# Kernel optimization log

Hardware: AMD Instinct MI355X
Metric: run time of the kernel (lower is better)

Reference implementation:

```python
import jax, jax.numpy as jnp
import numpy as np

N_NODES = 100000
N_EDGES = 3200000
IN_DIM = 64
HID = 64


def setup_inputs() -> dict:
    key = jax.random.key(0)
    ks = jax.random.split(key, 12)
    x = jax.random.normal(ks[0], (N_NODES, IN_DIM), dtype=jnp.float32)
    edge_index = jax.random.randint(ks[1], (2, N_EDGES), 0, N_NODES, dtype=jnp.int64)
    tau = jax.random.uniform(ks[2], (N_NODES, 1), dtype=jnp.float32)
    d1 = IN_DIM + 1  # augmented feature dim
    s1 = 1.0 / np.sqrt(d1)
    s2 = 1.0 / np.sqrt(HID)
    # SAGEConv: out = lin_l(mean_aggr) + lin_r(x); bias lives in lin_l. Weights stored [in, out].
    W1l = jax.random.uniform(ks[3], (d1, HID), jnp.float32, -s1, s1)
    b1l = jax.random.uniform(ks[4], (HID,), jnp.float32, -s1, s1)
    W1r = jax.random.uniform(ks[5], (d1, HID), jnp.float32, -s1, s1)
    W2l = jax.random.uniform(ks[6], (HID, HID), jnp.float32, -s2, s2)
    b2l = jax.random.uniform(ks[7], (HID,), jnp.float32, -s2, s2)
    W2r = jax.random.uniform(ks[8], (HID, HID), jnp.float32, -s2, s2)
    Wfc = jax.random.uniform(ks[9], (HID, 1), jnp.float32, -s2, s2)
    bfc = jax.random.uniform(ks[10], (1,), jnp.float32, -s2, s2)
    return {"x": x, "edge_index": edge_index, "tau": tau,
            "W1l": W1l, "b1l": b1l, "W1r": W1r,
            "W2l": W2l, "b2l": b2l, "W2r": W2r,
            "Wfc": Wfc, "bfc": bfc}


def _sage_conv(x, src, dst, Wl, bl, Wr, n_nodes):
    # mean aggregation of source-node features onto target nodes
    summed = jax.ops.segment_sum(x[src], dst, num_segments=n_nodes)  # [N, d]
    deg = jax.ops.segment_sum(jnp.ones(src.shape[0], x.dtype), dst, num_segments=n_nodes)
    mean = summed / jnp.maximum(deg, 1.0)[:, None]
    return mean @ Wl + bl + x @ Wr


def reference(x, edge_index, tau, W1l, b1l, W1r, W2l, b2l, W2r, Wfc, bfc):
    src, dst = edge_index[0], edge_index[1]
    n = x.shape[0]
    h = jnp.concatenate([x, tau], axis=1)  # augment_features: append tau column
    h = jax.nn.relu(_sage_conv(h, src, dst, W1l, b1l, W1r, n))
    h = jax.nn.relu(_sage_conv(h, src, dst, W2l, b2l, W2r, n))
    return h @ Wfc + bfc  # [N, 1]
```

## Files before the change

### kernel.cpp

```cpp
#include <hip/hip_runtime.h>
#include <hip/hip_bf16.h>
#include <hip/hip_fp16.h>
#include <hip/hip_fp8.h>


#define BSH 7
#define NBKT 782
#define NBLK 512
#define PER 6250
#define CAP 6144
#define ABLK 512

typedef _Float16 half8 __attribute__((ext_vector_type(8)));
typedef float floatx4 __attribute__((ext_vector_type(4)));
typedef float floatx2 __attribute__((ext_vector_type(2)));

struct h4s { __half2 lo, hi; };

#if __has_builtin(__builtin_amdgcn_cvt_pk_f32_fp8)
template <bool HI>
__device__ __forceinline__ float2 f8x2_to_f2(int v) {
    floatx2 r = __builtin_amdgcn_cvt_pk_f32_fp8(v, HI);
    return make_float2(r.x, r.y);
}
#else
template <bool HI>
__device__ __forceinline__ float2 f8x2_to_f2(int v) {
    unsigned short u = HI ? (unsigned short)(((unsigned)v) >> 16)
                          : (unsigned short)(v & 0xFFFF);
    __half2_raw r = __hip_cvt_fp8x2_to_halfraw2((__hip_fp8x2_storage_t)u, __HIP_E4M3);
    return __half22float2(*(__half2*)&r);
}
#endif

#if __has_builtin(__builtin_amdgcn_cvt_pk_fp8_f32)
__device__ __forceinline__ unsigned f4_to_f8x4(float a, float b, float c, float d) {
    int lo = __builtin_amdgcn_cvt_pk_fp8_f32(a, b, 0, false);
    return (unsigned)__builtin_amdgcn_cvt_pk_fp8_f32(c, d, lo, true);
}
__device__ __forceinline__ unsigned char f_to_f8(float a) {
    return (unsigned char)(__builtin_amdgcn_cvt_pk_fp8_f32(a, a, 0, false) & 0xFF);
}
#else
__device__ __forceinline__ unsigned f4_to_f8x4(float a, float b, float c, float d) {
    unsigned lo = (unsigned)__hip_cvt_float2_to_fp8x2(make_float2(a, b), __HIP_SATFINITE, __HIP_E4M3);
    unsigned hi = (unsigned)__hip_cvt_float2_to_fp8x2(make_float2(c, d), __HIP_SATFINITE, __HIP_E4M3);
    return lo | (hi << 16);
}
__device__ __forceinline__ unsigned char f_to_f8(float a) {
    return (unsigned char)__hip_cvt_float_to_fp8(a, __HIP_SATFINITE, __HIP_E4M3);
}
#endif

__global__ __launch_bounds__(256) void k_histprep(
    const int* __restrict__ dst, int* __restrict__ histT, int E,
    const float* __restrict__ x, __half* __restrict__ xh,
    unsigned char* __restrict__ xf8, int n4,
    const float* __restrict__ W1l, const float* __restrict__ W1r,
    const float* __restrict__ W2l, const float* __restrict__ W2r,
    __half* __restrict__ wbuf1, __half* __restrict__ wbuf2) {
    if (blockIdx.x < NBLK) {
        __shared__ int h[NBKT];
        for (int i = threadIdx.x; i < NBKT; i += 256) h[i] = 0;
        __syncthreads();
        int lo = blockIdx.x * PER;
        int hi = lo + PER; if (hi > E) hi = E;
        for (int e = lo + threadIdx.x; e < hi; e += 256)
            atomicAdd(&h[dst[e] >> BSH], 1);
        __syncthreads();
        for (int k = threadIdx.x; k < NBKT; k += 256)
            histT[k * NBLK + blockIdx.x] = h[k];
    } else if (blockIdx.x < NBLK + 9) {
        int idx = (blockIdx.x - NBLK) * 256 + threadIdx.x;
        if (idx < 1280) {
            int lane = idx & 63;
            int nt = (idx >> 6) & 3;
            int kstep = idx >> 8;
            int col = nt * 16 + (lane & 15);
            int kbase = kstep * 32 + (lane >> 4) * 8;
#pragma unroll
            for (int j = 0; j < 8; ++j) {
                int k = kbase + j;
                float v;
                if (k < 64)        v = W1l[k * 64 + col];
                else if (k < 128)  v = W1r[(k - 64) * 64 + col];
                else if (k == 128) v = W1l[64 * 64 + col];
                else if (k == 129) v = W1r[64 * 64 + col];
                else v = 0.f;
                wbuf1[(size_t)idx * 8 + j] = __float2half(v);
            }
        } else if (idx < 1280 + 1024) {
            int i2 = idx - 1280;
            int lane = i2 & 63;
            int nt = (i2 >> 6) & 3;
            int kstep = i2 >> 8;
            int col = nt * 16 + (lane & 15);
            int kbase = kstep * 32 + (lane >> 4) * 8;
#pragma unroll
            for (int j = 0; j < 8; ++j) {
                int k = kbase + j;
                float v = (k < 64) ? W2l[k * 64 + col] : W2r[(k - 64) * 64 + col];
                wbuf2[(size_t)i2 * 8 + j] = __float2half(v);
            }
        }
    } else {
        int i = (blockIdx.x - NBLK - 9) * 256 + threadIdx.x;
        if (i < n4) {
            float4 v = ((const float4*)x)[i];
            ((__half2*)xh)[2 * i]     = __floats2half2_rn(v.x, v.y);
            ((__half2*)xh)[2 * i + 1] = __floats2half2_rn(v.z, v.w);
            ((unsigned*)xf8)[i] = f4_to_f8x4(v.x, v.y, v.z, v.w);
        }
    }
}


__global__ __launch_bounds__(NBLK) void k_scanblk(int* __restrict__ histT,
                                                  int* __restrict__ btot) {
    __shared__ int s[NBLK];
    int k = blockIdx.x, t = threadIdx.x;
    int v = histT[k * NBLK + t];
    s[t] = v;
    __syncthreads();
    for (int off = 1; off < NBLK; off <<= 1) {
        int u = (t >= off) ? s[t - off] : 0;
        __syncthreads();
        s[t] += u;
        __syncthreads();
    }
    histT[k * NBLK + t] = s[t] - v;
    if (t == NBLK - 1) btot[k] = s[t];
}

__global__ __launch_bounds__(1024) void k_scanbkt(const int* __restrict__ btot,
                                                  int* __restrict__ bstart) {
    __shared__ int s[1024];
    int t = threadIdx.x;
    int v = (t < NBKT) ? btot[t] : 0;
    s[t] = v;
    __syncthreads();
    for (int off = 1; off < 1024; off <<= 1) {
        int u = (t >= off) ? s[t - off] : 0;
        __syncthreads();
        s[t] += u;
        __syncthreads();
    }
    if (t < NBKT) bstart[t] = s[t] - v;
    if (t == NBKT - 1) bstart[NBKT] = s[t];
}

__global__ __launch_bounds__(256) void k_scatter(const int* __restrict__ src,
                                                 const int* __restrict__ dst,
                                                 const int* __restrict__ histT,
                                                 const int* __restrict__ bstart,
                                                 int* __restrict__ binned, int E) {
    __shared__ int sorted[PER];
    __shared__ int lstart[NBKT + 1];
    __shared__ int cur[NBKT];
    __shared__ int gst[NBKT];
    __shared__ int tsum[256];
    int b = blockIdx.x, t = threadIdx.x;
    int base = b * PER;
    int blen = E - base; if (blen > PER) blen = PER;

    for (int k = t; k < NBKT; k += 256) lstart[k] = 0;
    __syncthreads();
    for (int e = base + t; e < base + blen; e += 256)
        atomicAdd(&lstart[dst[e] >> BSH], 1);
    __syncthreads();
    int c0 = 0;
    int i0 = t * 4;
#pragma unroll
    for (int j = 0; j < 4; ++j)
        if (i0 + j < NBKT) c0 += lstart[i0 + j];
    tsum[t] = c0;
    __syncthreads();
    for (int off = 1; off < 256; off <<= 1) {
        int u = (t >= off) ? tsum[t - off] : 0;
        __syncthreads();
        tsum[t] += u;
        __syncthreads();
    }
    int running = tsum[t] - c0;
    __syncthreads();
#pragma unroll
    for (int j = 0; j < 4; ++j) {
        int i = i0 + j;
        if (i < NBKT) {
            int v = lstart[i];
            lstart[i] = running;
            running += v;
        }
    }
    __syncthreads();
    if (t == 0) lstart[NBKT] = blen;
    for (int k = t; k < NBKT; k += 256) {
        cur[k] = lstart[k];
        gst[k] = bstart[k] + histT[k * NBLK + b];
    }
    __syncthreads();
    for (int e = base + t; e < base + blen; e += 256) {
        int d = dst[e], s = src[e];
        int pos = atomicAdd(&cur[d >> BSH], 1);
        sorted[pos] = (s << BSH) | (d & ((1 << BSH) - 1));
    }
    __syncthreads();
    int qw = t >> 4, ql = t & 15;
    for (int k = qw; k < NBKT; k += 16) {
        int st = lstart[k];
        int ln = lstart[k + 1] - st;
        int gd = gst[k];
        for (int i = ql; i < ln; i += 16)
            binned[gd + i] = sorted[st + i];
    }
}


__global__ __launch_bounds__(ABLK) void k_aggrb1(
    const int* __restrict__ binned, const int* __restrict__ bstart,
    const unsigned char* __restrict__ xf8, const float* __restrict__ tau,
    __half* __restrict__ zm1, __half* __restrict__ mt1, int N) {
    __shared__ int cidx[CAP];
    __shared__ int cnt[128], s[128], cur[128];
    int k = blockIdx.x, t = threadIdx.x;
    int lo = bstart[k], hi = bstart[k + 1];
    if (t < 128) cnt[t] = 0;
    __syncthreads();
    for (int e = lo + t; e < hi; e += ABLK)
        atomicAdd(&cnt[binned[e] & 127], 1);
    __syncthreads();
    if (t < 128) s[t] = cnt[t];
    __syncthreads();
    for (int off = 1; off < 128; off <<= 1) {
        int u = 0;
        if (t < 128 && t >= off) u = s[t - off];
        __syncthreads();
        if (t < 128) s[t] += u;
        __syncthreads();
    }
    if (t < 128) cur[t] = s[t] - cnt[t];
    __syncthreads();
    for (int e = lo + t; e < hi; e += ABLK) {
        int p = binned[e];
        int pos = atomicAdd(&cur[p & 127], 1);
        if (pos < CAP) cidx[pos] = p >> BSH;
    }
    __syncthreads();

    int lane = t & 63;
    int q = lane >> 4;
    int c = lane & 15;
    int qb = lane & 48;
    int g = c & 3;
    int ch = c >> 2;
    unsigned cb = (unsigned)(ch << 4);
    int bpl = (qb + g) << 2;
    const char* xb = (const char*)xf8;

    for (int p = (t >> 6); p < 32; p += (ABLK / 64)) {
        int ld = (p << 2) + q;
        int node = (k << BSH) + ld;
        int d = cnt[ld];
        int startL = cur[ld] - d;
        int dm = d;
        dm = max(dm, __shfl_xor(dm, 16, 64));
        dm = max(dm, __shfl_xor(dm, 32, 64));
        float4 A0 = {0.f, 0.f, 0.f, 0.f}, A1 = A0, A2 = A0, A3 = A0;
        float sumtau = 0.f;
        for (int base = 0; base < dm; base += 16) {
            int n = d - base;
            n = (n < 0) ? 0 : (n > 16 ? 16 : n);
            int nmax = dm - base; if (nmax > 16) nmax = 16;
            int ng = (nmax + 3) >> 2;
            int sidx = 0;
            if (c < n) {
                int ii = startL + base + c;
                if (ii >= CAP) ii = 0;
                sidx = cidx[ii];
                sumtau += tau[sidx];
            }
            int4 r0, r1, r2, r3;
            int i0 = __builtin_amdgcn_ds_bpermute(bpl, sidx);
            r0 = *(const int4*)(xb + (((unsigned)i0 << 6) + cb));
            if (ng > 1) {
                int i1 = __builtin_amdgcn_ds_bpermute(bpl + 16, sidx);
                r1 = *(const int4*)(xb + (((unsigned)i1 << 6) + cb));
            }
            if (ng > 2) {
                int i2 = __builtin_amdgcn_ds_bpermute(bpl + 32, sidx);
                r2 = *(const int4*)(xb + (((unsigned)i2 << 6) + cb));
            }
            if (ng > 3) {
                int i3 = __builtin_amdgcn_ds_bpermute(bpl + 48, sidx);
                r3 = *(const int4*)(xb + (((unsigned)i3 << 6) + cb));
            }
            auto accum = [&](const int4& r) {
                float2 l0 = f8x2_to_f2<false>(r.x), h0 = f8x2_to_f2<true>(r.x);
                float2 l1 = f8x2_to_f2<false>(r.y), h1v = f8x2_to_f2<true>(r.y);
                float2 l2 = f8x2_to_f2<false>(r.z), h2v = f8x2_to_f2<true>(r.z);
                float2 l3 = f8x2_to_f2<false>(r.w), h3v = f8x2_to_f2<true>(r.w);
                A0.x += l0.x; A0.y += l0.y; A0.z += h0.x; A0.w += h0.y;
                A1.x += l1.x; A1.y += l1.y; A1.z += h1v.x; A1.w += h1v.y;
                A2.x += l2.x; A2.y += l2.y; A2.z += h2v.x; A2.w += h2v.y;
                A3.x += l3.x; A3.y += l3.y; A3.z += h3v.x; A3.w += h3v.y;
            };
            if (g < n)                accum(r0);
            if (ng > 1 && 4 + g < n)  accum(r1);
            if (ng > 2 && 8 + g < n)  accum(r2);
            if (ng > 3 && 12 + g < n) accum(r3);
        }
#pragma unroll
        for (int off = 1; off <= 2; off <<= 1) {
            A0.x += __shfl_xor(A0.x, off, 64); A0.y += __shfl_xor(A0.y, off, 64);
            A0.z += __shfl_xor(A0.z, off, 64); A0.w += __shfl_xor(A0.w, off, 64);
            A1.x += __shfl_xor(A1.x, off, 64); A1.y += __shfl_xor(A1.y, off, 64);
            A1.z += __shfl_xor(A1.z, off, 64); A1.w += __shfl_xor(A1.w, off, 64);
            A2.x += __shfl_xor(A2.x, off, 64); A2.y += __shfl_xor(A2.y, off, 64);
            A2.z += __shfl_xor(A2.z, off, 64); A2.w += __shfl_xor(A2.w, off, 64);
            A3.x += __shfl_xor(A3.x, off, 64); A3.y += __shfl_xor(A3.y, off, 64);
            A3.z += __shfl_xor(A3.z, off, 64); A3.w += __shfl_xor(A3.w, off, 64);
        }
#pragma unroll
        for (int off = 8; off > 0; off >>= 1) sumtau += __shfl_xor(sumtau, off, 64);

        float inv = 1.f / fmaxf((float)d, 1.f);
        if (node < N) {
            float4 Aw = (g == 0) ? A0 : ((g == 1) ? A1 : ((g == 2) ? A2 : A3));
            h4s o;
            o.lo = __floats2half2_rn(Aw.x * inv, Aw.y * inv);
            o.hi = __floats2half2_rn(Aw.z * inv, Aw.w * inv);
            *(h4s*)(zm1 + (size_t)node * 64 + (ch << 4) + (g << 2)) = o;
            if (c == 0) mt1[node] = __float2half(sumtau * inv);
        }
    }
}

__global__ __launch_bounds__(ABLK) void k_aggrb2(
    const int* __restrict__ binned, const int* __restrict__ bstart,
    const unsigned char* __restrict__ h1f8, __half* __restrict__ zm2, int N) {
    __shared__ int cidx[CAP];
    __shared__ int cnt[128], s[128], cur[128];
    int k = blockIdx.x, t = threadIdx.x;
    int lo = bstart[k], hi = bstart[k + 1];
    if (t < 128) cnt[t] = 0;
    __syncthreads();
    for (int e = lo + t; e < hi; e += ABLK)
        atomicAdd(&cnt[binned[e] & 127], 1);
    __syncthreads();
    if (t < 128) s[t] = cnt[t];
    __syncthreads();
    for (int off = 1; off < 128; off <<= 1) {
        int u = 0;
        if (t < 128 && t >= off) u = s[t - off];
        __syncthreads();
        if (t < 128) s[t] += u;
        __syncthreads();
    }
    if (t < 128) cur[t] = s[t] - cnt[t];
    __syncthreads();
    for (int e = lo + t; e < hi; e += ABLK) {
        int p = binned[e];
        int pos = atomicAdd(&cur[p & 127], 1);
        if (pos < CAP) cidx[pos] = p >> BSH;
    }
    __syncthreads();

    int lane = t & 63;
    int q = lane >> 4;
    int c = lane & 15;
    int qb = lane & 48;
    int g = c & 3;
    int ch = c >> 2;
    unsigned cb = (unsigned)(ch << 4);
    int bpl = (qb + g) << 2;
    const char* hb = (const char*)h1f8;

    for (int p = (t >> 6); p < 32; p += (ABLK / 64)) {
        int ld = (p << 2) + q;
        int node = (k << BSH) + ld;
        int d = cnt[ld];
        int startL = cur[ld] - d;
        int dm = d;
        dm = max(dm, __shfl_xor(dm, 16, 64));
        dm = max(dm, __shfl_xor(dm, 32, 64));
        float4 A0 = {0.f, 0.f, 0.f, 0.f}, A1 = A0, A2 = A0, A3 = A0;
        for (int base = 0; base < dm; base += 16) {
            int n = d - base;
            n = (n < 0) ? 0 : (n > 16 ? 16 : n);
            int nmax = dm - base; if (nmax > 16) nmax = 16;
            int ng = (nmax + 3) >> 2;
            int sidx = 0;
            if (c < n) {
                int ii = startL + base + c;
                if (ii >= CAP) ii = 0;
                sidx = cidx[ii];
            }
            int4 r0, r1, r2, r3;
            int i0 = __builtin_amdgcn_ds_bpermute(bpl, sidx);
            r0 = *(const int4*)(hb + (((unsigned)i0 << 6) + cb));
            if (ng > 1) {
                int i1 = __builtin_amdgcn_ds_bpermute(bpl + 16, sidx);
                r1 = *(const int4*)(hb + (((unsigned)i1 << 6) + cb));
            }
            if (ng > 2) {
                int i2 = __builtin_amdgcn_ds_bpermute(bpl + 32, sidx);
                r2 = *(const int4*)(hb + (((unsigned)i2 << 6) + cb));
            }
            if (ng > 3) {
                int i3 = __builtin_amdgcn_ds_bpermute(bpl + 48, sidx);
                r3 = *(const int4*)(hb + (((unsigned)i3 << 6) + cb));
            }
            auto accum = [&](const int4& r) {
                float2 l0 = f8x2_to_f2<false>(r.x), h0 = f8x2_to_f2<true>(r.x);
                float2 l1 = f8x2_to_f2<false>(r.y), h1v = f8x2_to_f2<true>(r.y);
                float2 l2 = f8x2_to_f2<false>(r.z), h2v = f8x2_to_f2<true>(r.z);
                float2 l3 = f8x2_to_f2<false>(r.w), h3v = f8x2_to_f2<true>(r.w);
                A0.x += l0.x; A0.y += l0.y; A0.z += h0.x; A0.w += h0.y;
                A1.x += l1.x; A1.y += l1.y; A1.z += h1v.x; A1.w += h1v.y;
                A2.x += l2.x; A2.y += l2.y; A2.z += h2v.x; A2.w += h2v.y;
                A3.x += l3.x; A3.y += l3.y; A3.z += h3v.x; A3.w += h3v.y;
            };
            if (g < n)                accum(r0);
            if (ng > 1 && 4 + g < n)  accum(r1);
            if (ng > 2 && 8 + g < n)  accum(r2);
            if (ng > 3 && 12 + g < n) accum(r3);
        }
#pragma unroll
        for (int off = 1; off <= 2; off <<= 1) {
            A0.x += __shfl_xor(A0.x, off, 64); A0.y += __shfl_xor(A0.y, off, 64);
            A0.z += __shfl_xor(A0.z, off, 64); A0.w += __shfl_xor(A0.w, off, 64);
            A1.x += __shfl_xor(A1.x, off, 64); A1.y += __shfl_xor(A1.y, off, 64);
            A1.z += __shfl_xor(A1.z, off, 64); A1.w += __shfl_xor(A1.w, off, 64);
            A2.x += __shfl_xor(A2.x, off, 64); A2.y += __shfl_xor(A2.y, off, 64);
            A2.z += __shfl_xor(A2.z, off, 64); A2.w += __shfl_xor(A2.w, off, 64);
            A3.x += __shfl_xor(A3.x, off, 64); A3.y += __shfl_xor(A3.y, off, 64);
            A3.z += __shfl_xor(A3.z, off, 64); A3.w += __shfl_xor(A3.w, off, 64);
        }
        float inv = 1.f / fmaxf((float)d, 1.f);
        if (node < N) {
            float4 Aw = (g == 0) ? A0 : ((g == 1) ? A1 : ((g == 2) ? A2 : A3));
            h4s o;
            o.lo = __floats2half2_rn(Aw.x * inv, Aw.y * inv);
            o.hi = __floats2half2_rn(Aw.z * inv, Aw.w * inv);
            *(h4s*)(zm2 + (size_t)node * 64 + (ch << 4) + (g << 2)) = o;
        }
    }
}


__global__ __launch_bounds__(256) void k_gemm1(
    const __half* __restrict__ zm1, const __half* __restrict__ mt1,
    const __half* __restrict__ xh, const float* __restrict__ tau,
    const __half* __restrict__ wbuf1, const float* __restrict__ b1l,
    __half* __restrict__ h1, unsigned char* __restrict__ h1f8, int ntiles) {
    int tile = blockIdx.x * 4 + (threadIdx.x >> 6);
    if (tile >= ntiles) return;
    int lane = threadIdx.x & 63;
    int sub = lane & 15;
    int quad = lane >> 4;
    int row = tile * 16 + sub;

    floatx4 acc0 = {0.f, 0.f, 0.f, 0.f};
    floatx4 acc1 = {0.f, 0.f, 0.f, 0.f};
    floatx4 acc2 = {0.f, 0.f, 0.f, 0.f};
    floatx4 acc3 = {0.f, 0.f, 0.f, 0.f};

    const _Float16* zrow = (const _Float16*)zm1 + (size_t)row * 64 + quad * 8;
    const _Float16* xrow = (const _Float16*)xh + (size_t)row * 64 + quad * 8;
    const _Float16* wb = (const _Float16*)wbuf1 + (size_t)lane * 8;

    half8 amat[5];
    amat[0] = *(const half8*)(zrow);
    amat[1] = *(const half8*)(zrow + 32);
    amat[2] = *(const half8*)(xrow);
    amat[3] = *(const half8*)(xrow + 32);
    half8 a4 = {0, 0, 0, 0, 0, 0, 0, 0};
    if (quad == 0) {
        a4[0] = ((const _Float16*)mt1)[row];
        a4[1] = (_Float16)tau[row];
    }
    amat[4] = a4;

#pragma unroll
    for (int ks = 0; ks < 5; ++ks) {
        half8 a = amat[ks];
        half8 b0 = *(const half8*)(wb + (size_t)(ks * 4 + 0) * 512);
        half8 b1 = *(const half8*)(wb + (size_t)(ks * 4 + 1) * 512);
        half8 b2 = *(const half8*)(wb + (size_t)(ks * 4 + 2) * 512);
        half8 b3 = *(const half8*)(wb + (size_t)(ks * 4 + 3) * 512);
        acc0 = __builtin_amdgcn_mfma_f32_16x16x32_f16(a, b0, acc0, 0, 0, 0);
        acc1 = __builtin_amdgcn_mfma_f32_16x16x32_f16(a, b1, acc1, 0, 0, 0);
        acc2 = __builtin_amdgcn_mfma_f32_16x16x32_f16(a, b2, acc2, 0, 0, 0);
        acc3 = __builtin_amdgcn_mfma_f32_16x16x32_f16(a, b3, acc3, 0, 0, 0);
    }
    float bv0 = b1l[sub], bv1 = b1l[16 + sub], bv2 = b1l[32 + sub], bv3 = b1l[48 + sub];
#pragma unroll
    for (int reg = 0; reg < 4; ++reg) {
        int r = quad * 4 + reg;
        float v0 = fmaxf(acc0[reg] + bv0, 0.f);
        float v1 = fmaxf(acc1[reg] + bv1, 0.f);
        float v2 = fmaxf(acc2[reg] + bv2, 0.f);
        float v3 = fmaxf(acc3[reg] + bv3, 0.f);
        __half* orow = h1 + (size_t)(tile * 16 + r) * 64;
        orow[sub]      = __float2half(v0);
        orow[16 + sub] = __float2half(v1);
        orow[32 + sub] = __float2half(v2);
        orow[48 + sub] = __float2half(v3);
        unsigned char* orow8 = h1f8 + (size_t)(tile * 16 + r) * 64;
        orow8[sub]      = f_to_f8(v0);
        orow8[16 + sub] = f_to_f8(v1);
        orow8[32 + sub] = f_to_f8(v2);
        orow8[48 + sub] = f_to_f8(v3);
    }
}

__global__ __launch_bounds__(256) void k_gemm2(
    const __half* __restrict__ zm2, const __half* __restrict__ h1,
    const __half* __restrict__ wbuf2, const float* __restrict__ b2l,
    const float* __restrict__ Wfc, const float* __restrict__ bfc,
    float* __restrict__ out, int ntiles) {
    int tile = blockIdx.x * 4 + (threadIdx.x >> 6);
    if (tile >= ntiles) return;
    int lane = threadIdx.x & 63;
    int sub = lane & 15;
    int quad = lane >> 4;
    int row = tile * 16 + sub;

    floatx4 acc0 = {0.f, 0.f, 0.f, 0.f};
    floatx4 acc1 = {0.f, 0.f, 0.f, 0.f};
    floatx4 acc2 = {0.f, 0.f, 0.f, 0.f};
    floatx4 acc3 = {0.f, 0.f, 0.f, 0.f};

    const _Float16* zrow = (const _Float16*)zm2 + (size_t)row * 64 + quad * 8;
    const _Float16* hrow = (const _Float16*)h1 + (size_t)row * 64 + quad * 8;
    const _Float16* wb = (const _Float16*)wbuf2 + (size_t)lane * 8;

    half8 amat[4];
    amat[0] = *(const half8*)(zrow);
    amat[1] = *(const half8*)(zrow + 32);
    amat[2] = *(const half8*)(hrow);
    amat[3] = *(const half8*)(hrow + 32);

#pragma unroll
    for (int ks = 0; ks < 4; ++ks) {
        half8 a = amat[ks];
        half8 b0 = *(const half8*)(wb + (size_t)(ks * 4 + 0) * 512);
        half8 b1 = *(const half8*)(wb + (size_t)(ks * 4 + 1) * 512);
        half8 b2 = *(const half8*)(wb + (size_t)(ks * 4 + 2) * 512);
        half8 b3 = *(const half8*)(wb + (size_t)(ks * 4 + 3) * 512);
        acc0 = __builtin_amdgcn_mfma_f32_16x16x32_f16(a, b0, acc0, 0, 0, 0);
        acc1 = __builtin_amdgcn_mfma_f32_16x16x32_f16(a, b1, acc1, 0, 0, 0);
        acc2 = __builtin_amdgcn_mfma_f32_16x16x32_f16(a, b2, acc2, 0, 0, 0);
        acc3 = __builtin_amdgcn_mfma_f32_16x16x32_f16(a, b3, acc3, 0, 0, 0);
    }
    float bb0 = b2l[sub], bb1 = b2l[16 + sub], bb2 = b2l[32 + sub], bb3 = b2l[48 + sub];
    float wv0 = Wfc[sub], wv1 = Wfc[16 + sub], wv2 = Wfc[32 + sub], wv3 = Wfc[48 + sub];
    float p[4];
#pragma unroll
    for (int reg = 0; reg < 4; ++reg) {
        p[reg] = fmaxf(acc0[reg] + bb0, 0.f) * wv0
               + fmaxf(acc1[reg] + bb1, 0.f) * wv1
               + fmaxf(acc2[reg] + bb2, 0.f) * wv2
               + fmaxf(acc3[reg] + bb3, 0.f) * wv3;
    }
#pragma unroll
    for (int m = 1; m <= 8; m <<= 1) {
#pragma unroll
        for (int reg = 0; reg < 4; ++reg) p[reg] += __shfl_xor(p[reg], m, 64);
    }
    if (sub == 0) {
        float b0 = bfc[0];
#pragma unroll
        for (int reg = 0; reg < 4; ++reg)
            out[tile * 16 + quad * 4 + reg] = p[reg] + b0;
    }
}

extern "C" void kernel_launch(void* const* d_in, const int* in_sizes, int n_in,
                              void* d_out, int out_size, void* d_ws, size_t ws_size,
                              hipStream_t stream) {
    const float* x   = (const float*)d_in[0];
    const int*   ei  = (const int*)d_in[1];
    const float* tau = (const float*)d_in[2];
    const float* W1l = (const float*)d_in[3];
    const float* b1l = (const float*)d_in[4];
    const float* W1r = (const float*)d_in[5];
    const float* W2l = (const float*)d_in[6];
    const float* b2l = (const float*)d_in[7];
    const float* W2r = (const float*)d_in[8];
    const float* Wfc = (const float*)d_in[9];
    const float* bfc = (const float*)d_in[10];
    float* out = (float*)d_out;

    const int N = in_sizes[0] / 64;
    const int E = in_sizes[1] / 2;
    const int* src = ei;
    const int* dst = ei + E;

    char* w = (char*)d_ws;
    auto take = [&](size_t b) { char* p = w; w += (b + 255) & ~(size_t)255; return p; };
    int*           histT  = (int*)take((size_t)NBKT * NBLK * 4);
    int*           btot   = (int*)take((size_t)NBKT * 4);
    int*           bstart = (int*)take((size_t)(NBKT + 1) * 4);
    int*           binned = (int*)take((size_t)E * 4);
    __half*        xh     = (__half*)take((size_t)N * 64 * 2);
    unsigned char* xf8    = (unsigned char*)take((size_t)N * 64);
    __half*        h1     = (__half*)take((size_t)N * 64 * 2);
    unsigned char* h1f8   = (unsigned char*)take((size_t)N * 64);
    __half*        zm1    = (__half*)take((size_t)N * 64 * 2);
    __half*        mt1    = (__half*)take((size_t)N * 2);
    __half*        zm2    = (__half*)take((size_t)N * 64 * 2);
    __half*        wbuf1  = (__half*)take(1280 * 8 * 2);
    __half*        wbuf2  = (__half*)take(1024 * 8 * 2);

    int n4 = N * 16;
    int hpblocks = NBLK + 9 + (n4 + 255) / 256;
    int ntiles = N / 16;
    int gblocks = (ntiles + 3) / 4;

    k_histprep<<<hpblocks, 256, 0, stream>>>(dst, histT, E, x, xh, xf8, n4,
                                             W1l, W1r, W2l, W2r, wbuf1, wbuf2);
    k_scanblk <<<NBKT, NBLK, 0, stream>>>(histT, btot);
    k_scanbkt <<<1, 1024, 0, stream>>>(btot, bstart);
    k_scatter <<<NBLK, 256, 0, stream>>>(src, dst, histT, bstart, binned, E);
    k_aggrb1  <<<NBKT, ABLK, 0, stream>>>(binned, bstart, xf8, tau, zm1, mt1, N);
    k_gemm1   <<<gblocks, 256, 0, stream>>>(zm1, mt1, xh, tau, wbuf1, b1l, h1, h1f8, ntiles);
    k_aggrb2  <<<NBKT, ABLK, 0, stream>>>(binned, bstart, h1f8, zm2, N);
    k_gemm2   <<<gblocks, 256, 0, stream>>>(zm2, h1, wbuf2, b2l, Wfc, bfc, out, ntiles);
}
```

Baseline: 276.8 us.

## Split each aggregation bucket across two half-blocks and drop bpermute index broadcast

Each 128-node bucket in both aggregation kernels is now handled by two 256-thread blocks, each taking 64 nodes and keeping a smaller shared index buffer. This gives more, smaller blocks for load balance and occupancy. The cost is that both blocks scan the full bucket edge list and filter by node half. Lanes now read their neighbour indices straight from shared memory instead of through a ds_bpermute broadcast, and the tau sum is done by the first column group with a shorter shuffle reduction.

```diff
diff --git a/kernel.cpp b/kernel.cpp
--- a/kernel.cpp
+++ b/kernel.cpp
@@ -8,8 +8,8 @@
 #define NBKT 782
 #define NBLK 512
 #define PER 6250
-#define CAP 6144
-#define ABLK 512
+#define CAPH 3072
+#define AB2 256
 
 typedef _Float16 half8 __attribute__((ext_vector_type(8)));
 typedef float floatx4 __attribute__((ext_vector_type(4)));
@@ -216,50 +216,52 @@
 }
 
 
-__global__ __launch_bounds__(ABLK) void k_aggrb1(
+__global__ __launch_bounds__(AB2) void k_aggrb1(
     const int* __restrict__ binned, const int* __restrict__ bstart,
     const unsigned char* __restrict__ xf8, const float* __restrict__ tau,
     __half* __restrict__ zm1, __half* __restrict__ mt1, int N) {
-    __shared__ int cidx[CAP];
-    __shared__ int cnt[128], s[128], cur[128];
-    int k = blockIdx.x, t = threadIdx.x;
+    __shared__ int cidx[CAPH];
+    __shared__ int cnt[64], s[64], cur[64];
+    int k = blockIdx.x >> 1, h = blockIdx.x & 1, t = threadIdx.x;
     int lo = bstart[k], hi = bstart[k + 1];
-    if (t < 128) cnt[t] = 0;
-    __syncthreads();
-    for (int e = lo + t; e < hi; e += ABLK)
-        atomicAdd(&cnt[binned[e] & 127], 1);
-    __syncthreads();
-    if (t < 128) s[t] = cnt[t];
-    __syncthreads();
-    for (int off = 1; off < 128; off <<= 1) {
+    if (t < 64) cnt[t] = 0;
+    __syncthreads();
+    for (int e = lo + t; e < hi; e += AB2) {
+        int p = binned[e];
+        if (((p >> 6) & 1) == h) atomicAdd(&cnt[p & 63], 1);
+    }
+    __syncthreads();
+    if (t < 64) s[t] = cnt[t];
+    __syncthreads();
+    for (int off = 1; off < 64; off <<= 1) {
         int u = 0;
-        if (t < 128 && t >= off) u = s[t - off];
-        __syncthreads();
-        if (t < 128) s[t] += u;
-        __syncthreads();
-    }
-    if (t < 128) cur[t] = s[t] - cnt[t];
-    __syncthreads();
-    for (int e = lo + t; e < hi; e += ABLK) {
+        if (t < 64 && t >= off) u = s[t - off];
+        __syncthreads();
+        if (t < 64) s[t] += u;
+        __syncthreads();
+    }
+    if (t < 64) cur[t] = s[t] - cnt[t];
+    __syncthreads();
+    for (int e = lo + t; e < hi; e += AB2) {
         int p = binned[e];
-        int pos = atomicAdd(&cur[p & 127], 1);
-        if (pos < CAP) cidx[pos] = p >> BSH;
+        if (((p >> 6) & 1) == h) {
+            int pos = atomicAdd(&cur[p & 63], 1);
+            if (pos < CAPH) cidx[pos] = p >> BSH;
+        }
     }
     __syncthreads();
 
     int lane = t & 63;
     int q = lane >> 4;
     int c = lane & 15;
-    int qb = lane & 48;
     int g = c & 3;
     int ch = c >> 2;
     unsigned cb = (unsigned)(ch << 4);
-    int bpl = (qb + g) << 2;
     const char* xb = (const char*)xf8;
 
-    for (int p = (t >> 6); p < 32; p += (ABLK / 64)) {
+    for (int p = (t >> 6); p < 16; p += (AB2 / 64)) {
         int ld = (p << 2) + q;
-        int node = (k << BSH) + ld;
+        int node = (k << BSH) + (h << 6) + ld;
         int d = cnt[ld];
         int startL = cur[ld] - d;
         int dm = d;
@@ -268,31 +270,32 @@
         float4 A0 = {0.f, 0.f, 0.f, 0.f}, A1 = A0, A2 = A0, A3 = A0;
         float sumtau = 0.f;
         for (int base = 0; base < dm; base += 16) {
-            int n = d - base;
-            n = (n < 0) ? 0 : (n > 16 ? 16 : n);
             int nmax = dm - base; if (nmax > 16) nmax = 16;
             int ng = (nmax + 3) >> 2;
-            int sidx = 0;
-            if (c < n) {
-                int ii = startL + base + c;
-                if (ii >= CAP) ii = 0;
-                sidx = cidx[ii];
-                sumtau += tau[sidx];
-            }
+            int s0 = base + g;
+            int s1 = s0 + 4, s2 = s0 + 8, s3 = s0 + 12;
+            bool v0 = s0 < d, v1 = s1 < d, v2 = s2 < d, v3 = s3 < d;
+            int sx0, sx1, sx2, sx3;
             int4 r0, r1, r2, r3;
-            int i0 = __builtin_amdgcn_ds_bpermute(bpl, sidx);
-            r0 = *(const int4*)(xb + (((unsigned)i0 << 6) + cb));
+            sx0 = cidx[v0 ? startL + s0 : 0];
+            r0 = *(const int4*)(xb + (((unsigned)sx0 << 6) + cb));
             if (ng > 1) {
-                int i1 = __builtin_amdgcn_ds_bpermute(bpl + 16, sidx);
-                r1 = *(const int4*)(xb + (((unsigned)i1 << 6) + cb));
+                sx1 = cidx[v1 ? startL + s1 : 0];
+                r1 = *(const int4*)(xb + (((unsigned)sx1 << 6) + cb));
             }
             if (ng > 2) {
-                int i2 = __builtin_amdgcn_ds_bpermute(bpl + 32, sidx);
-                r2 = *(const int4*)(xb + (((unsigned)i2 << 6) + cb));
+                sx2 = cidx[v2 ? startL + s2 : 0];
+                r2 = *(const int4*)(xb + (((unsigned)sx2 << 6) + cb));
             }
             if (ng > 3) {
-                int i3 = __builtin_amdgcn_ds_bpermute(bpl + 48, sidx);
-                r3 = *(const int4*)(xb + (((unsigned)i3 << 6) + cb));
+                sx3 = cidx[v3 ? startL + s3 : 0];
+                r3 = *(const int4*)(xb + (((unsigned)sx3 << 6) + cb));
+            }
+            if (ch == 0) {
+                if (v0) sumtau += tau[sx0];
+                if (ng > 1 && v1) sumtau += tau[sx1];
+                if (ng > 2 && v2) sumtau += tau[sx2];
+                if (ng > 3 && v3) sumtau += tau[sx3];
             }
             auto accum = [&](const int4& r) {
                 float2 l0 = f8x2_to_f2<false>(r.x), h0 = f8x2_to_f2<true>(r.x);
@@ -304,10 +307,10 @@
                 A2.x += l2.x; A2.y += l2.y; A2.z += h2v.x; A2.w += h2v.y;
                 A3.x += l3.x; A3.y += l3.y; A3.z += h3v.x; A3.w += h3v.y;
             };
-            if (g < n)                accum(r0);
-            if (ng > 1 && 4 + g < n)  accum(r1);
-            if (ng > 2 && 8 + g < n)  accum(r2);
-            if (ng > 3 && 12 + g < n) accum(r3);
+            if (v0)            accum(r0);
+            if (ng > 1 && v1)  accum(r1);
+            if (ng > 2 && v2)  accum(r2);
+            if (ng > 3 && v3)  accum(r3);
         }
 #pragma unroll
         for (int off = 1; off <= 2; off <<= 1) {
@@ -319,10 +322,8 @@
             A2.z += __shfl_xor(A2.z, off, 64); A2.w += __shfl_xor(A2.w, off, 64);
             A3.x += __shfl_xor(A3.x, off, 64); A3.y += __shfl_xor(A3.y, off, 64);
             A3.z += __shfl_xor(A3.z, off, 64); A3.w += __shfl_xor(A3.w, off, 64);
-        }
-#pragma unroll
-        for (int off = 8; off > 0; off >>= 1) sumtau += __shfl_xor(sumtau, off, 64);
-
+            sumtau += __shfl_xor(sumtau, off, 64);
+        }
         float inv = 1.f / fmaxf((float)d, 1.f);
         if (node < N) {
             float4 Aw = (g == 0) ? A0 : ((g == 1) ? A1 : ((g == 2) ? A2 : A3));
@@ -335,49 +336,51 @@
     }
 }
 
-__global__ __launch_bounds__(ABLK) void k_aggrb2(
+__global__ __launch_bounds__(AB2) void k_aggrb2(
     const int* __restrict__ binned, const int* __restrict__ bstart,
     const unsigned char* __restrict__ h1f8, __half* __restrict__ zm2, int N) {
-    __shared__ int cidx[CAP];
-    __shared__ int cnt[128], s[128], cur[128];
-    int k = blockIdx.x, t = threadIdx.x;
+    __shared__ int cidx[CAPH];
+    __shared__ int cnt[64], s[64], cur[64];
+    int k = blockIdx.x >> 1, h = blockIdx.x & 1, t = threadIdx.x;
     int lo = bstart[k], hi = bstart[k + 1];
-    if (t < 128) cnt[t] = 0;
-    __syncthreads();
-    for (int e = lo + t; e < hi; e += ABLK)
-        atomicAdd(&cnt[binned[e] & 127], 1);
-    __syncthreads();
-    if (t < 128) s[t] = cnt[t];
-    __syncthreads();
-    for (int off = 1; off < 128; off <<= 1) {
+    if (t < 64) cnt[t] = 0;
+    __syncthreads();
+    for (int e = lo + t; e < hi; e += AB2) {
+        int p = binned[e];
+        if (((p >> 6) & 1) == h) atomicAdd(&cnt[p & 63], 1);
+    }
+    __syncthreads();
+    if (t < 64) s[t] = cnt[t];
+    __syncthreads();
+    for (int off = 1; off < 64; off <<= 1) {
         int u = 0;
-        if (t < 128 && t >= off) u = s[t - off];
-        __syncthreads();
-        if (t < 128) s[t] += u;
-        __syncthreads();
-    }
-    if (t < 128) cur[t] = s[t] - cnt[t];
-    __syncthreads();
-    for (int e = lo + t; e < hi; e += ABLK) {
+        if (t < 64 && t >= off) u = s[t - off];
+        __syncthreads();
+        if (t < 64) s[t] += u;
+        __syncthreads();
+    }
+    if (t < 64) cur[t] = s[t] - cnt[t];
+    __syncthreads();
+    for (int e = lo + t; e < hi; e += AB2) {
         int p = binned[e];
-        int pos = atomicAdd(&cur[p & 127], 1);
-        if (pos < CAP) cidx[pos] = p >> BSH;
+        if (((p >> 6) & 1) == h) {
+            int pos = atomicAdd(&cur[p & 63], 1);
+            if (pos < CAPH) cidx[pos] = p >> BSH;
+        }
     }
     __syncthreads();
 
     int lane = t & 63;
     int q = lane >> 4;
     int c = lane & 15;
-    int qb = lane & 48;
     int g = c & 3;
     int ch = c >> 2;
     unsigned cb = (unsigned)(ch << 4);
-    int bpl = (qb + g) << 2;
     const char* hb = (const char*)h1f8;
 
-    for (int p = (t >> 6); p < 32; p += (ABLK / 64)) {
+    for (int p = (t >> 6); p < 16; p += (AB2 / 64)) {
         int ld = (p << 2) + q;
-        int node = (k << BSH) + ld;
+        int node = (k << BSH) + (h << 6) + ld;
         int d = cnt[ld];
         int startL = cur[ld] - d;
         int dm = d;
@@ -385,30 +388,26 @@
         dm = max(dm, __shfl_xor(dm, 32, 64));
         float4 A0 = {0.f, 0.f, 0.f, 0.f}, A1 = A0, A2 = A0, A3 = A0;
         for (int base = 0; base < dm; base += 16) {
-            int n = d - base;
-            n = (n < 0) ? 0 : (n > 16 ? 16 : n);
             int nmax = dm - base; if (nmax > 16) nmax = 16;
             int ng = (nmax + 3) >> 2;
-            int sidx = 0;
-            if (c < n) {
-                int ii = startL + base + c;
-                if (ii >= CAP) ii = 0;
-                sidx = cidx[ii];
-            }
+            int s0 = base + g;
+            int s1 = s0 + 4, s2 = s0 + 8, s3 = s0 + 12;
+            bool v0 = s0 < d, v1 = s1 < d, v2 = s2 < d, v3 = s3 < d;
+            int sx0, sx1, sx2, sx3;
             int4 r0, r1, r2, r3;
-            int i0 = __builtin_amdgcn_ds_bpermute(bpl, sidx);
-            r0 = *(const int4*)(hb + (((unsigned)i0 << 6) + cb));
+            sx0 = cidx[v0 ? startL + s0 : 0];
+            r0 = *(const int4*)(hb + (((unsigned)sx0 << 6) + cb));
             if (ng > 1) {
-                int i1 = __builtin_amdgcn_ds_bpermute(bpl + 16, sidx);
-                r1 = *(const int4*)(hb + (((unsigned)i1 << 6) + cb));
+                sx1 = cidx[v1 ? startL + s1 : 0];
+                r1 = *(const int4*)(hb + (((unsigned)sx1 << 6) + cb));
             }
             if (ng > 2) {
-                int i2 = __builtin_amdgcn_ds_bpermute(bpl + 32, sidx);
-                r2 = *(const int4*)(hb + (((unsigned)i2 << 6) + cb));
+                sx2 = cidx[v2 ? startL + s2 : 0];
+                r2 = *(const int4*)(hb + (((unsigned)sx2 << 6) + cb));
             }
             if (ng > 3) {
-                int i3 = __builtin_amdgcn_ds_bpermute(bpl + 48, sidx);
-                r3 = *(const int4*)(hb + (((unsigned)i3 << 6) + cb));
+                sx3 = cidx[v3 ? startL + s3 : 0];
+                r3 = *(const int4*)(hb + (((unsigned)sx3 << 6) + cb));
             }
             auto accum = [&](const int4& r) {
                 float2 l0 = f8x2_to_f2<false>(r.x), h0 = f8x2_to_f2<true>(r.x);
@@ -420,10 +419,10 @@
                 A2.x += l2.x; A2.y += l2.y; A2.z += h2v.x; A2.w += h2v.y;
                 A3.x += l3.x; A3.y += l3.y; A3.z += h3v.x; A3.w += h3v.y;
             };
-            if (g < n)                accum(r0);
-            if (ng > 1 && 4 + g < n)  accum(r1);
-            if (ng > 2 && 8 + g < n)  accum(r2);
-            if (ng > 3 && 12 + g < n) accum(r3);
+            if (v0)            accum(r0);
+            if (ng > 1 && v1)  accum(r1);
+            if (ng > 2 && v2)  accum(r2);
+            if (ng > 3 && v3)  accum(r3);
         }
 #pragma unroll
         for (int off = 1; off <= 2; off <<= 1) {
@@ -623,8 +622,8 @@
     k_scanblk <<<NBKT, NBLK, 0, stream>>>(histT, btot);
     k_scanbkt <<<1, 1024, 0, stream>>>(btot, bstart);
     k_scatter <<<NBLK, 256, 0, stream>>>(src, dst, histT, bstart, binned, E);
-    k_aggrb1  <<<NBKT, ABLK, 0, stream>>>(binned, bstart, xf8, tau, zm1, mt1, N);
+    k_aggrb1  <<<2 * NBKT, AB2, 0, stream>>>(binned, bstart, xf8, tau, zm1, mt1, N);
     k_gemm1   <<<gblocks, 256, 0, stream>>>(zm1, mt1, xh, tau, wbuf1, b1l, h1, h1f8, ntiles);
-    k_aggrb2  <<<NBKT, ABLK, 0, stream>>>(binned, bstart, h1f8, zm2, N);
+    k_aggrb2  <<<2 * NBKT, AB2, 0, stream>>>(binned, bstart, h1f8, zm2, N);
     k_gemm2   <<<gblocks, 256, 0, stream>>>(zm2, h1, wbuf2, b2l, Wfc, bfc, out, ntiles);
 }
```

After: 267.3 us. 3.4% less time.
